# Performance work log

Measured on AMD Instinct MI355X. Metric: run time of the kernel, lower is better.

The kernel has to match this reference:

```python
import jax, jax.numpy as jnp
import numpy as np

B, T, F, H = 1024, 512, 64, 128


def setup_inputs() -> dict:
    key = jax.random.key(0)
    ks = jax.random.split(key, 9)
    s_ih = 1.0 / np.sqrt(H)
    inp = {
        "x": jax.random.normal(ks[0], (B, T, F), dtype=jnp.float32),
        # PyTorch GRU packed weights: [3H, F] and [3H, H], gate order (r, z, n)
        "W_ih": jax.random.uniform(ks[1], (3 * H, F), minval=-s_ih, maxval=s_ih, dtype=jnp.float32),
        "W_hh": jax.random.uniform(ks[2], (3 * H, H), minval=-s_ih, maxval=s_ih, dtype=jnp.float32),
        "b_ih": jax.random.uniform(ks[3], (3 * H,), minval=-s_ih, maxval=s_ih, dtype=jnp.float32),
        "b_hh": jax.random.uniform(ks[4], (3 * H,), minval=-s_ih, maxval=s_ih, dtype=jnp.float32),
        "W1": jax.random.uniform(ks[5], (32, H), minval=-1 / np.sqrt(H), maxval=1 / np.sqrt(H), dtype=jnp.float32),
        "b1": jax.random.uniform(ks[6], (32,), minval=-1 / np.sqrt(H), maxval=1 / np.sqrt(H), dtype=jnp.float32),
        "W2": jax.random.uniform(ks[7], (1, 32), minval=-1 / np.sqrt(32), maxval=1 / np.sqrt(32), dtype=jnp.float32),
        "b2": jax.random.uniform(ks[8], (1,), minval=-1 / np.sqrt(32), maxval=1 / np.sqrt(32), dtype=jnp.float32),
    }
    return inp


def _gru_last_hidden(x, W_ih, W_hh, b_ih, b_hh):
    # Precompute input-side gate pre-activations for all timesteps: [B, T, 3H]
    xg = jnp.einsum("btf,gf->btg", x, W_ih) + b_ih
    h0 = jnp.zeros((x.shape[0], W_hh.shape[1]), dtype=x.dtype)

    def step(h, xg_t):
        hg = h @ W_hh.T + b_hh  # [B, 3H]
        xr, xz, xn = jnp.split(xg_t, 3, axis=-1)
        hr, hz, hn = jnp.split(hg, 3, axis=-1)
        r = jax.nn.sigmoid(xr + hr)
        z = jax.nn.sigmoid(xz + hz)
        n = jnp.tanh(xn + r * hn)
        h_new = (1.0 - z) * n + z * h
        return h_new, None

    hT, _ = jax.lax.scan(step, h0, jnp.swapaxes(xg, 0, 1))  # scan over T
    return hT  # [B, H]


def reference(x, W_ih, W_hh, b_ih, b_hh, W1, b1, W2, b2):
    hT = _gru_last_hidden(x, W_ih, W_hh, b_ih, b_hh)
    hidden = jax.nn.relu(hT @ W1.T + b1)  # [B, 32]; dropout is identity at inference
    out = hidden @ W2.T + b2  # [B, 1]
    return out.squeeze(-1)  # [B]
```

## Files before the change

kernel.cpp:

```cpp
#include <hip/hip_runtime.h>
#include <math.h>


#define Bsz  1024
#define Tlen 512
#define Fdim 64
#define Hdim 128
#define Gdim 384
#define NB   16
#define NTHR 512
#define NBLK (Bsz / NB)

typedef __attribute__((ext_vector_type(8))) _Float16 f16x8;
typedef __attribute__((ext_vector_type(4))) _Float16 f16x4;
typedef __attribute__((ext_vector_type(2))) _Float16 f16x2;
typedef __attribute__((ext_vector_type(4))) float    f32x4;

__device__ __forceinline__ float fast_sigmoid(float v) {
    return __builtin_amdgcn_rcpf(1.f + __expf(-v));
}
__device__ __forceinline__ float fast_tanh(float v) {
    return 1.f - 2.f * __builtin_amdgcn_rcpf(__expf(2.f * v) + 1.f);
}

__global__ void
__attribute__((amdgpu_flat_work_group_size(NTHR, NTHR), amdgpu_waves_per_eu(2, 2)))
gru_mfma(const float* __restrict__ x,
         const float* __restrict__ W_ih, const float* __restrict__ W_hh,
         const float* __restrict__ b_ih, const float* __restrict__ b_hh,
         const float* __restrict__ W1, const float* __restrict__ b1,
         const float* __restrict__ W2, const float* __restrict__ b2,
         float* __restrict__ out)
{
    __shared__ __align__(16) _Float16 WH[24 * 4 * 4 * 128];
    __shared__ __align__(16) _Float16 WI[24 * 2 * 4 * 128];
    __shared__ __align__(16) _Float16 U0[6 * 4 * 16 * 8];
    __shared__ __align__(16) _Float16 U1[6 * 4 * 16 * 8];

    const int tid  = threadIdx.x;
    const int w    = tid >> 6;
    const int l    = tid & 63;
    const int q    = l >> 4;
    const int bcol = l & 15;
    const int b0   = blockIdx.x * NB;

    for (int i = tid; i < Gdim * Hdim; i += NTHR) {
        int gr = i >> 7, k = i & 127;
        int idx = (((gr >> 4) * 4 + (k >> 5)) * 4 + ((k & 31) >> 3)) * 128
                + (gr & 15) * 8 + (k & 7);
        WH[idx] = (_Float16)W_hh[i];
    }
    for (int i = tid; i < Gdim * Fdim; i += NTHR) {
        int gr = i >> 6, k = i & 63;
        int idx = (((gr >> 4) * 2 + (k >> 5)) * 4 + ((k & 31) >> 3)) * 128
                + (gr & 15) * 8 + (k & 7);
        WI[idx] = (_Float16)W_ih[i];
    }
    for (int i = tid; i < 2048; i += NTHR) U0[i] = (_Float16)0.f;
    {
        int e = tid * 2, bx_ = e >> 6, j = e & 63;
        float2 xv = *reinterpret_cast<const float2*>(
            &x[((size_t)(b0 + bx_) * Tlen + 0) * Fdim + j]);
        int kk = 128 + j;
        int idx = (((kk >> 5) * 4 + ((kk & 31) >> 3)) * 16 + bx_) * 8 + (kk & 7);
        U0[idx]     = (_Float16)xv.x;
        U0[idx + 1] = (_Float16)xv.y;
    }

    float br[4], bz[4], bnh[4], bnx[4];
    #pragma unroll
    for (int j = 0; j < 4; ++j) {
        int gr = 16 * w + q * 4 + j;
        br[j]  = b_ih[gr] + b_hh[gr];
        bz[j]  = b_ih[Hdim + gr] + b_hh[Hdim + gr];
        bnh[j] = b_hh[2 * Hdim + gr];
        bnx[j] = b_ih[2 * Hdim + gr];
    }

    float hp0 = 0.f, hp1 = 0.f, hp2 = 0.f, hp3 = 0.f;

    const int kb    = 16 * w + 4 * q;
    const int hbase = (((kb >> 5) * 4 + ((kb & 31) >> 3)) * 16 + bcol) * 8 + (kb & 7);

    const int e_x = tid * 2, bx = e_x >> 6, jx = e_x & 63;
    const int kx  = 128 + jx;
    const int xidx = (((kx >> 5) * 4 + ((kx & 31) >> 3)) * 16 + bx) * 8 + (kx & 7);
    const float* xsrc = &x[(size_t)(b0 + bx) * Tlen * Fdim + jx];

    __syncthreads();

#define WHF(gt, kt) (*reinterpret_cast<const f16x8*>(&WH[((((gt)*4+(kt))*4+q)*128) + (l&15)*8]))
#define WIF(gt, kt) (*reinterpret_cast<const f16x8*>(&WI[((((gt)*2+(kt))*4+q)*128) + (l&15)*8]))
#define MFMA(a, b, c) __builtin_amdgcn_mfma_f32_16x16x32_f16((a), (b), (c), 0, 0, 0)

    f16x8 whr0 = WHF(w, 0),      whr1 = WHF(w, 1),      whr2 = WHF(w, 2),      whr3 = WHF(w, 3);
    f16x8 whz0 = WHF(8 + w, 0),  whz1 = WHF(8 + w, 1),  whz2 = WHF(8 + w, 2),  whz3 = WHF(8 + w, 3);
    f16x8 whn0 = WHF(16 + w, 0), whn1 = WHF(16 + w, 1), whn2 = WHF(16 + w, 2), whn3 = WHF(16 + w, 3);
    f16x8 wir0 = WIF(w, 0),      wir1 = WIF(w, 1);
    f16x8 wiz0 = WIF(8 + w, 0),  wiz1 = WIF(8 + w, 1);
    f16x8 win0 = WIF(16 + w, 0), win1 = WIF(16 + w, 1);

    float2 xp = *reinterpret_cast<const float2*>(xsrc + (size_t)1 * Fdim);

    auto step = [&](const _Float16* __restrict__ Ur, _Float16* __restrict__ Uw, int t) {
        asm volatile("" : "+v"(whr0), "+v"(whr1), "+v"(whr2), "+v"(whr3),
                          "+v"(whz0), "+v"(whz1));
        asm volatile("" : "+v"(whz2), "+v"(whz3), "+v"(whn0), "+v"(whn1),
                          "+v"(whn2), "+v"(whn3));
        asm volatile("" : "+v"(wir0), "+v"(wir1), "+v"(wiz0), "+v"(wiz1),
                          "+v"(win0), "+v"(win1));

        f16x8 ub0 = *reinterpret_cast<const f16x8*>(&Ur[((0*4+q)*16 + bcol)*8]);
        f16x8 ub1 = *reinterpret_cast<const f16x8*>(&Ur[((1*4+q)*16 + bcol)*8]);
        f16x8 ub2 = *reinterpret_cast<const f16x8*>(&Ur[((2*4+q)*16 + bcol)*8]);
        f16x8 ub3 = *reinterpret_cast<const f16x8*>(&Ur[((3*4+q)*16 + bcol)*8]);
        f16x8 ub4 = *reinterpret_cast<const f16x8*>(&Ur[((4*4+q)*16 + bcol)*8]);
        f16x8 ub5 = *reinterpret_cast<const f16x8*>(&Ur[((5*4+q)*16 + bcol)*8]);

        float2 xw = xp;
        if (t + 2 < Tlen)
            xp = *reinterpret_cast<const float2*>(xsrc + (size_t)(t + 2) * Fdim);

        f32x4 cr  = {br[0],  br[1],  br[2],  br[3]};
        f32x4 cz  = {bz[0],  bz[1],  bz[2],  bz[3]};
        f32x4 cnh = {bnh[0], bnh[1], bnh[2], bnh[3]};
        f32x4 cnx = {bnx[0], bnx[1], bnx[2], bnx[3]};

        cr  = MFMA(whr0, ub0, cr);
        cz  = MFMA(whz0, ub0, cz);
        cnh = MFMA(whn0, ub0, cnh);
        cr  = MFMA(whr1, ub1, cr);
        cz  = MFMA(whz1, ub1, cz);
        cnh = MFMA(whn1, ub1, cnh);
        cr  = MFMA(whr2, ub2, cr);
        cz  = MFMA(whz2, ub2, cz);
        cnh = MFMA(whn2, ub2, cnh);
        cr  = MFMA(whr3, ub3, cr);
        cz  = MFMA(whz3, ub3, cz);
        cnh = MFMA(whn3, ub3, cnh);
        cr  = MFMA(wir0, ub4, cr);
        cz  = MFMA(wiz0, ub4, cz);
        cnx = MFMA(win0, ub4, cnx);
        cr  = MFMA(wir1, ub5, cr);
        cz  = MFMA(wiz1, ub5, cz);
        cnx = MFMA(win1, ub5, cnx);

        float r0 = fast_sigmoid(cr[0]), z0 = fast_sigmoid(cz[0]);
        float r1 = fast_sigmoid(cr[1]), z1 = fast_sigmoid(cz[1]);
        float r2 = fast_sigmoid(cr[2]), z2 = fast_sigmoid(cz[2]);
        float r3 = fast_sigmoid(cr[3]), z3 = fast_sigmoid(cz[3]);
        float n0 = fast_tanh(cnx[0] + r0 * cnh[0]);
        float n1 = fast_tanh(cnx[1] + r1 * cnh[1]);
        float n2 = fast_tanh(cnx[2] + r2 * cnh[2]);
        float n3 = fast_tanh(cnx[3] + r3 * cnh[3]);
        hp0 = (1.f - z0) * n0 + z0 * hp0;
        hp1 = (1.f - z1) * n1 + z1 * hp1;
        hp2 = (1.f - z2) * n2 + z2 * hp2;
        hp3 = (1.f - z3) * n3 + z3 * hp3;

        f16x4 hq = {(_Float16)hp0, (_Float16)hp1, (_Float16)hp2, (_Float16)hp3};
        *reinterpret_cast<f16x4*>(&Uw[hbase]) = hq;

        if (t + 1 < Tlen) {
            f16x2 xq = {(_Float16)xw.x, (_Float16)xw.y};
            *reinterpret_cast<f16x2*>(&Uw[xidx]) = xq;
        }
        __syncthreads();
    };

    #pragma unroll 1
    for (int t = 0; t < Tlen; t += 2) {
        step(U0, U1, t);
        step(U1, U0, t + 1);
    }

    {
        int m = tid & 31, b = tid >> 5;
        float acc = b1[m];
        #pragma unroll 8
        for (int k = 0; k < Hdim; ++k) {
            int ui = (((k >> 5) * 4 + ((k & 31) >> 3)) * 16 + b) * 8 + (k & 7);
            acc += W1[m * Hdim + k] * (float)U0[ui];
        }
        float v = W2[m] * fmaxf(acc, 0.f);
        v += __shfl_xor(v, 1,  32);
        v += __shfl_xor(v, 2,  32);
        v += __shfl_xor(v, 4,  32);
        v += __shfl_xor(v, 8,  32);
        v += __shfl_xor(v, 16, 32);
        if (m == 0) out[b0 + b] = v + b2[0];
    }
}

extern "C" void kernel_launch(void* const* d_in, const int* in_sizes, int n_in,
                              void* d_out, int out_size, void* d_ws, size_t ws_size,
                              hipStream_t stream)
{
    const float* x    = (const float*)d_in[0];
    const float* W_ih = (const float*)d_in[1];
    const float* W_hh = (const float*)d_in[2];
    const float* b_ih = (const float*)d_in[3];
    const float* b_hh = (const float*)d_in[4];
    const float* W1   = (const float*)d_in[5];
    const float* b1   = (const float*)d_in[6];
    const float* W2   = (const float*)d_in[7];
    const float* b2   = (const float*)d_in[8];
    float* out = (float*)d_out;

    dim3 grid(NBLK), block(NTHR);
    hipLaunchKernelGGL(gru_mfma, grid, block, 0, stream,
                       x, W_ih, W_hh, b_ih, b_hh, W1, b1, W2, b2, out);
}
```

Measured before the change: 331.3 us.

## Halve block to 4 waves, each computing two gate tiles with AGPR-held weights

Shrinks the workgroup from 8 to 4 waves, so each wave computes two 16-row gate tiles per timestep (36 MFMAs instead of 18). The recurrent weights are pinned in AGPRs to make room for the doubled register footprint, and x loads are widened to float4. The aim is to cut the per-step barrier cost and wave-scheduling overhead of the serial recurrence by using fewer, more MFMA-dense waves. The trade-off is a longer serial MFMA chain per wave and lower occupancy (waves_per_eu 1), which could lengthen each step.

```diff
diff --git a/kernel.cpp b/kernel.cpp
--- a/kernel.cpp
+++ b/kernel.cpp
@@ -8,12 +8,11 @@
 #define Hdim 128
 #define Gdim 384
 #define NB   16
-#define NTHR 512
+#define NTHR 256
 #define NBLK (Bsz / NB)
 
 typedef __attribute__((ext_vector_type(8))) _Float16 f16x8;
 typedef __attribute__((ext_vector_type(4))) _Float16 f16x4;
-typedef __attribute__((ext_vector_type(2))) _Float16 f16x2;
 typedef __attribute__((ext_vector_type(4))) float    f32x4;
 
 __device__ __forceinline__ float fast_sigmoid(float v) {
@@ -24,7 +23,7 @@
 }
 
 __global__ void
-__attribute__((amdgpu_flat_work_group_size(NTHR, NTHR), amdgpu_waves_per_eu(2, 2)))
+__attribute__((amdgpu_flat_work_group_size(NTHR, NTHR), amdgpu_waves_per_eu(1, 1)))
 gru_mfma(const float* __restrict__ x,
          const float* __restrict__ W_ih, const float* __restrict__ W_hh,
          const float* __restrict__ b_ih, const float* __restrict__ b_hh,
@@ -58,31 +57,38 @@
     }
     for (int i = tid; i < 2048; i += NTHR) U0[i] = (_Float16)0.f;
     {
-        int e = tid * 2, bx_ = e >> 6, j = e & 63;
-        float2 xv = *reinterpret_cast<const float2*>(
+        int e = tid * 4, bx_ = e >> 6, j = e & 63;
+        float4 xv = *reinterpret_cast<const float4*>(
             &x[((size_t)(b0 + bx_) * Tlen + 0) * Fdim + j]);
         int kk = 128 + j;
         int idx = (((kk >> 5) * 4 + ((kk & 31) >> 3)) * 16 + bx_) * 8 + (kk & 7);
-        U0[idx]     = (_Float16)xv.x;
-        U0[idx + 1] = (_Float16)xv.y;
-    }
-
-    float br[4], bz[4], bnh[4], bnx[4];
-    #pragma unroll
-    for (int j = 0; j < 4; ++j) {
-        int gr = 16 * w + q * 4 + j;
-        br[j]  = b_ih[gr] + b_hh[gr];
-        bz[j]  = b_ih[Hdim + gr] + b_hh[Hdim + gr];
-        bnh[j] = b_hh[2 * Hdim + gr];
-        bnx[j] = b_ih[2 * Hdim + gr];
-    }
-
-    float hp0 = 0.f, hp1 = 0.f, hp2 = 0.f, hp3 = 0.f;
-
-    const int kb    = 16 * w + 4 * q;
-    const int hbase = (((kb >> 5) * 4 + ((kb & 31) >> 3)) * 16 + bcol) * 8 + (kb & 7);
-
-    const int e_x = tid * 2, bx = e_x >> 6, jx = e_x & 63;
+        f16x4 xq = {(_Float16)xv.x, (_Float16)xv.y, (_Float16)xv.z, (_Float16)xv.w};
+        *reinterpret_cast<f16x4*>(&U0[idx]) = xq;
+    }
+
+#define GR(S, J) (16 * (2 * w + (S)) + 4 * q + (J))
+    f32x4 brv0 = {b_ih[GR(0,0)] + b_hh[GR(0,0)], b_ih[GR(0,1)] + b_hh[GR(0,1)],
+                  b_ih[GR(0,2)] + b_hh[GR(0,2)], b_ih[GR(0,3)] + b_hh[GR(0,3)]};
+    f32x4 brv1 = {b_ih[GR(1,0)] + b_hh[GR(1,0)], b_ih[GR(1,1)] + b_hh[GR(1,1)],
+                  b_ih[GR(1,2)] + b_hh[GR(1,2)], b_ih[GR(1,3)] + b_hh[GR(1,3)]};
+    f32x4 bzv0 = {b_ih[Hdim+GR(0,0)] + b_hh[Hdim+GR(0,0)], b_ih[Hdim+GR(0,1)] + b_hh[Hdim+GR(0,1)],
+                  b_ih[Hdim+GR(0,2)] + b_hh[Hdim+GR(0,2)], b_ih[Hdim+GR(0,3)] + b_hh[Hdim+GR(0,3)]};
+    f32x4 bzv1 = {b_ih[Hdim+GR(1,0)] + b_hh[Hdim+GR(1,0)], b_ih[Hdim+GR(1,1)] + b_hh[Hdim+GR(1,1)],
+                  b_ih[Hdim+GR(1,2)] + b_hh[Hdim+GR(1,2)], b_ih[Hdim+GR(1,3)] + b_hh[Hdim+GR(1,3)]};
+    f32x4 bnhv0 = {b_hh[2*Hdim+GR(0,0)], b_hh[2*Hdim+GR(0,1)], b_hh[2*Hdim+GR(0,2)], b_hh[2*Hdim+GR(0,3)]};
+    f32x4 bnhv1 = {b_hh[2*Hdim+GR(1,0)], b_hh[2*Hdim+GR(1,1)], b_hh[2*Hdim+GR(1,2)], b_hh[2*Hdim+GR(1,3)]};
+    f32x4 bnxv0 = {b_ih[2*Hdim+GR(0,0)], b_ih[2*Hdim+GR(0,1)], b_ih[2*Hdim+GR(0,2)], b_ih[2*Hdim+GR(0,3)]};
+    f32x4 bnxv1 = {b_ih[2*Hdim+GR(1,0)], b_ih[2*Hdim+GR(1,1)], b_ih[2*Hdim+GR(1,2)], b_ih[2*Hdim+GR(1,3)]};
+
+    float hp00 = 0.f, hp01 = 0.f, hp02 = 0.f, hp03 = 0.f;
+    float hp10 = 0.f, hp11 = 0.f, hp12 = 0.f, hp13 = 0.f;
+
+    const int kb0 = 16 * (2 * w + 0) + 4 * q;
+    const int kb1 = 16 * (2 * w + 1) + 4 * q;
+    const int hbase0 = (((kb0 >> 5) * 4 + ((kb0 & 31) >> 3)) * 16 + bcol) * 8 + (kb0 & 7);
+    const int hbase1 = (((kb1 >> 5) * 4 + ((kb1 & 31) >> 3)) * 16 + bcol) * 8 + (kb1 & 7);
+
+    const int e_x = tid * 4, bx = e_x >> 6, jx = e_x & 63;
     const int kx  = 128 + jx;
     const int xidx = (((kx >> 5) * 4 + ((kx & 31) >> 3)) * 16 + bx) * 8 + (kx & 7);
     const float* xsrc = &x[(size_t)(b0 + bx) * Tlen * Fdim + jx];
@@ -93,22 +99,32 @@
 #define WIF(gt, kt) (*reinterpret_cast<const f16x8*>(&WI[((((gt)*2+(kt))*4+q)*128) + (l&15)*8]))
 #define MFMA(a, b, c) __builtin_amdgcn_mfma_f32_16x16x32_f16((a), (b), (c), 0, 0, 0)
 
-    f16x8 whr0 = WHF(w, 0),      whr1 = WHF(w, 1),      whr2 = WHF(w, 2),      whr3 = WHF(w, 3);
-    f16x8 whz0 = WHF(8 + w, 0),  whz1 = WHF(8 + w, 1),  whz2 = WHF(8 + w, 2),  whz3 = WHF(8 + w, 3);
-    f16x8 whn0 = WHF(16 + w, 0), whn1 = WHF(16 + w, 1), whn2 = WHF(16 + w, 2), whn3 = WHF(16 + w, 3);
-    f16x8 wir0 = WIF(w, 0),      wir1 = WIF(w, 1);
-    f16x8 wiz0 = WIF(8 + w, 0),  wiz1 = WIF(8 + w, 1);
-    f16x8 win0 = WIF(16 + w, 0), win1 = WIF(16 + w, 1);
-
-    float2 xp = *reinterpret_cast<const float2*>(xsrc + (size_t)1 * Fdim);
+    f16x8 whr00 = WHF(2*w,      0), whr01 = WHF(2*w,      1), whr02 = WHF(2*w,      2), whr03 = WHF(2*w,      3);
+    f16x8 whr10 = WHF(2*w+1,    0), whr11 = WHF(2*w+1,    1), whr12 = WHF(2*w+1,    2), whr13 = WHF(2*w+1,    3);
+    f16x8 whz00 = WHF(8+2*w,    0), whz01 = WHF(8+2*w,    1), whz02 = WHF(8+2*w,    2), whz03 = WHF(8+2*w,    3);
+    f16x8 whz10 = WHF(8+2*w+1,  0), whz11 = WHF(8+2*w+1,  1), whz12 = WHF(8+2*w+1,  2), whz13 = WHF(8+2*w+1,  3);
+    f16x8 whn00 = WHF(16+2*w,   0), whn01 = WHF(16+2*w,   1), whn02 = WHF(16+2*w,   2), whn03 = WHF(16+2*w,   3);
+    f16x8 whn10 = WHF(16+2*w+1, 0), whn11 = WHF(16+2*w+1, 1), whn12 = WHF(16+2*w+1, 2), whn13 = WHF(16+2*w+1, 3);
+    f16x8 wir00 = WIF(2*w,      0), wir01 = WIF(2*w,      1);
+    f16x8 wir10 = WIF(2*w+1,    0), wir11 = WIF(2*w+1,    1);
+    f16x8 wiz00 = WIF(8+2*w,    0), wiz01 = WIF(8+2*w,    1);
+    f16x8 wiz10 = WIF(8+2*w+1,  0), wiz11 = WIF(8+2*w+1,  1);
+    f16x8 win00 = WIF(16+2*w,   0), win01 = WIF(16+2*w,   1);
+    f16x8 win10 = WIF(16+2*w+1, 0), win11 = WIF(16+2*w+1, 1);
+
+    float4 xp = *reinterpret_cast<const float4*>(xsrc + (size_t)1 * Fdim);
 
     auto step = [&](const _Float16* __restrict__ Ur, _Float16* __restrict__ Uw, int t) {
-        asm volatile("" : "+v"(whr0), "+v"(whr1), "+v"(whr2), "+v"(whr3),
-                          "+v"(whz0), "+v"(whz1));
-        asm volatile("" : "+v"(whz2), "+v"(whz3), "+v"(whn0), "+v"(whn1),
-                          "+v"(whn2), "+v"(whn3));
-        asm volatile("" : "+v"(wir0), "+v"(wir1), "+v"(wiz0), "+v"(wiz1),
-                          "+v"(win0), "+v"(win1));
+        asm volatile("" : "+a"(whr00), "+a"(whr01), "+a"(whr02), "+a"(whr03),
+                          "+a"(whr10), "+a"(whr11), "+a"(whr12), "+a"(whr13));
+        asm volatile("" : "+a"(whz00), "+a"(whz01), "+a"(whz02), "+a"(whz03),
+                          "+a"(whz10), "+a"(whz11), "+a"(whz12), "+a"(whz13));
+        asm volatile("" : "+a"(whn00), "+a"(whn01), "+a"(whn02), "+a"(whn03),
+                          "+a"(whn10), "+a"(whn11), "+a"(whn12), "+a"(whn13));
+        asm volatile("" : "+v"(wir00), "+v"(wir01), "+v"(wir10), "+v"(wir11),
+                          "+v"(wiz00), "+v"(wiz01));
+        asm volatile("" : "+v"(wiz10), "+v"(wiz11), "+v"(win00), "+v"(win01),
+                          "+v"(win10), "+v"(win11));
 
         f16x8 ub0 = *reinterpret_cast<const f16x8*>(&Ur[((0*4+q)*16 + bcol)*8]);
         f16x8 ub1 = *reinterpret_cast<const f16x8*>(&Ur[((1*4+q)*16 + bcol)*8]);
@@ -117,53 +133,69 @@
         f16x8 ub4 = *reinterpret_cast<const f16x8*>(&Ur[((4*4+q)*16 + bcol)*8]);
         f16x8 ub5 = *reinterpret_cast<const f16x8*>(&Ur[((5*4+q)*16 + bcol)*8]);
 
-        float2 xw = xp;
+        float4 xw = xp;
         if (t + 2 < Tlen)
-            xp = *reinterpret_cast<const float2*>(xsrc + (size_t)(t + 2) * Fdim);
-
-        f32x4 cr  = {br[0],  br[1],  br[2],  br[3]};
-        f32x4 cz  = {bz[0],  bz[1],  bz[2],  bz[3]};
-        f32x4 cnh = {bnh[0], bnh[1], bnh[2], bnh[3]};
-        f32x4 cnx = {bnx[0], bnx[1], bnx[2], bnx[3]};
-
-        cr  = MFMA(whr0, ub0, cr);
-        cz  = MFMA(whz0, ub0, cz);
-        cnh = MFMA(whn0, ub0, cnh);
-        cr  = MFMA(whr1, ub1, cr);
-        cz  = MFMA(whz1, ub1, cz);
-        cnh = MFMA(whn1, ub1, cnh);
-        cr  = MFMA(whr2, ub2, cr);
-        cz  = MFMA(whz2, ub2, cz);
-        cnh = MFMA(whn2, ub2, cnh);
-        cr  = MFMA(whr3, ub3, cr);
-        cz  = MFMA(whz3, ub3, cz);
-        cnh = MFMA(whn3, ub3, cnh);
-        cr  = MFMA(wir0, ub4, cr);
-        cz  = MFMA(wiz0, ub4, cz);
-        cnx = MFMA(win0, ub4, cnx);
-        cr  = MFMA(wir1, ub5, cr);
-        cz  = MFMA(wiz1, ub5, cz);
-        cnx = MFMA(win1, ub5, cnx);
-
-        float r0 = fast_sigmoid(cr[0]), z0 = fast_sigmoid(cz[0]);
-        float r1 = fast_sigmoid(cr[1]), z1 = fast_sigmoid(cz[1]);
-        float r2 = fast_sigmoid(cr[2]), z2 = fast_sigmoid(cz[2]);
-        float r3 = fast_sigmoid(cr[3]), z3 = fast_sigmoid(cz[3]);
-        float n0 = fast_tanh(cnx[0] + r0 * cnh[0]);
-        float n1 = fast_tanh(cnx[1] + r1 * cnh[1]);
-        float n2 = fast_tanh(cnx[2] + r2 * cnh[2]);
-        float n3 = fast_tanh(cnx[3] + r3 * cnh[3]);
-        hp0 = (1.f - z0) * n0 + z0 * hp0;
-        hp1 = (1.f - z1) * n1 + z1 * hp1;
-        hp2 = (1.f - z2) * n2 + z2 * hp2;
-        hp3 = (1.f - z3) * n3 + z3 * hp3;
-
-        f16x4 hq = {(_Float16)hp0, (_Float16)hp1, (_Float16)hp2, (_Float16)hp3};
-        *reinterpret_cast<f16x4*>(&Uw[hbase]) = hq;
+            xp = *reinterpret_cast<const float4*>(xsrc + (size_t)(t + 2) * Fdim);
+
+        f32x4 cr0 = brv0, cr1 = brv1, cz0 = bzv0, cz1 = bzv1;
+        f32x4 cnh0 = bnhv0, cnh1 = bnhv1, cnx0 = bnxv0, cnx1 = bnxv1;
+
+        cr0 = MFMA(whr00, ub0, cr0);  cr1 = MFMA(whr10, ub0, cr1);
+        cz0 = MFMA(whz00, ub0, cz0);  cz1 = MFMA(whz10, ub0, cz1);
+        cnh0 = MFMA(whn00, ub0, cnh0); cnh1 = MFMA(whn10, ub0, cnh1);
+        cr0 = MFMA(whr01, ub1, cr0);  cr1 = MFMA(whr11, ub1, cr1);
+        cz0 = MFMA(whz01, ub1, cz0);  cz1 = MFMA(whz11, ub1, cz1);
+        cnh0 = MFMA(whn01, ub1, cnh0); cnh1 = MFMA(whn11, ub1, cnh1);
+        cr0 = MFMA(whr02, ub2, cr0);  cr1 = MFMA(whr12, ub2, cr1);
+        cz0 = MFMA(whz02, ub2, cz0);  cz1 = MFMA(whz12, ub2, cz1);
+        cnh0 = MFMA(whn02, ub2, cnh0); cnh1 = MFMA(whn12, ub2, cnh1);
+        cr0 = MFMA(whr03, ub3, cr0);  cr1 = MFMA(whr13, ub3, cr1);
+        cz0 = MFMA(whz03, ub3, cz0);  cz1 = MFMA(whz13, ub3, cz1);
+        cnh0 = MFMA(whn03, ub3, cnh0); cnh1 = MFMA(whn13, ub3, cnh1);
+        cr0 = MFMA(wir00, ub4, cr0);  cr1 = MFMA(wir10, ub4, cr1);
+        cz0 = MFMA(wiz00, ub4, cz0);  cz1 = MFMA(wiz10, ub4, cz1);
+        cnx0 = MFMA(win00, ub4, cnx0); cnx1 = MFMA(win10, ub4, cnx1);
+        cr0 = MFMA(wir01, ub5, cr0);  cr1 = MFMA(wir11, ub5, cr1);
+        cz0 = MFMA(wiz01, ub5, cz0);  cz1 = MFMA(wiz11, ub5, cz1);
+        cnx0 = MFMA(win01, ub5, cnx0); cnx1 = MFMA(win11, ub5, cnx1);
+
+        {
+            float r0 = fast_sigmoid(cr0[0]), z0 = fast_sigmoid(cz0[0]);
+            float r1 = fast_sigmoid(cr0[1]), z1 = fast_sigmoid(cz0[1]);
+            float r2 = fast_sigmoid(cr0[2]), z2 = fast_sigmoid(cz0[2]);
+            float r3 = fast_sigmoid(cr0[3]), z3 = fast_sigmoid(cz0[3]);
+            float n0 = fast_tanh(cnx0[0] + r0 * cnh0[0]);
+            float n1 = fast_tanh(cnx0[1] + r1 * cnh0[1]);
+            float n2 = fast_tanh(cnx0[2] + r2 * cnh0[2]);
+            float n3 = fast_tanh(cnx0[3] + r3 * cnh0[3]);
+            hp00 = (1.f - z0) * n0 + z0 * hp00;
+            hp01 = (1.f - z1) * n1 + z1 * hp01;
+            hp02 = (1.f - z2) * n2 + z2 * hp02;
+            hp03 = (1.f - z3) * n3 + z3 * hp03;
+        }
+        {
+            float r0 = fast_sigmoid(cr1[0]), z0 = fast_sigmoid(cz1[0]);
+            float r1 = fast_sigmoid(cr1[1]), z1 = fast_sigmoid(cz1[1]);
+            float r2 = fast_sigmoid(cr1[2]), z2 = fast_sigmoid(cz1[2]);
+            float r3 = fast_sigmoid(cr1[3]), z3 = fast_sigmoid(cz1[3]);
+            float n0 = fast_tanh(cnx1[0] + r0 * cnh1[0]);
+            float n1 = fast_tanh(cnx1[1] + r1 * cnh1[1]);
+            float n2 = fast_tanh(cnx1[2] + r2 * cnh1[2]);
+            float n3 = fast_tanh(cnx1[3] + r3 * cnh1[3]);
+            hp10 = (1.f - z0) * n0 + z0 * hp10;
+            hp11 = (1.f - z1) * n1 + z1 * hp11;
+            hp12 = (1.f - z2) * n2 + z2 * hp12;
+            hp13 = (1.f - z3) * n3 + z3 * hp13;
+        }
+
+        f16x4 hq0 = {(_Float16)hp00, (_Float16)hp01, (_Float16)hp02, (_Float16)hp03};
+        f16x4 hq1 = {(_Float16)hp10, (_Float16)hp11, (_Float16)hp12, (_Float16)hp13};
+        *reinterpret_cast<f16x4*>(&Uw[hbase0]) = hq0;
+        *reinterpret_cast<f16x4*>(&Uw[hbase1]) = hq1;
 
         if (t + 1 < Tlen) {
-            f16x2 xq = {(_Float16)xw.x, (_Float16)xw.y};
-            *reinterpret_cast<f16x2*>(&Uw[xidx]) = xq;
+            f16x4 xq = {(_Float16)xw.x, (_Float16)xw.y, (_Float16)xw.z, (_Float16)xw.w};
+            *reinterpret_cast<f16x4*>(&Uw[xidx]) = xq;
         }
         __syncthreads();
     };
@@ -174,8 +206,8 @@
         step(U1, U0, t + 1);
     }
 
-    {
-        int m = tid & 31, b = tid >> 5;
+    for (int sidx = tid; sidx < 512; sidx += NTHR) {
+        int m = sidx & 31, b = sidx >> 5;
         float acc = b1[m];
         #pragma unroll 8
         for (int k = 0; k < Hdim; ++k) {
```

After: 446.2 us. 1.35x slower.

## Load GRU weights directly to registers and use LDS-only step barrier

Applied to the files above, without the earlier changes.

Weight fragments are read from global memory and converted to fp16 directly into registers, removing the shared-memory staging of W_hh and W_ih and its setup barrier work. The per-timestep __syncthreads is replaced by an s_waitcnt lgkmcnt(0) plus s_barrier wrapped in scheduling barriers, so the step no longer waits on the outstanding global prefetch of the next x slice. The hidden update is rewritten as n + z*(h-n) to save an operation. Removing the register pinning asm may let the compiler reorder or spill weight registers, and the sched barriers constrain instruction scheduling.

```diff
diff --git a/kernel.cpp b/kernel.cpp
--- a/kernel.cpp
+++ b/kernel.cpp
@@ -22,6 +22,12 @@
 __device__ __forceinline__ float fast_tanh(float v) {
     return 1.f - 2.f * __builtin_amdgcn_rcpf(__expf(2.f * v) + 1.f);
 }
+
+#define BAR_LDS() do {                                                   \
+    __builtin_amdgcn_sched_barrier(0);                                   \
+    asm volatile("s_waitcnt lgkmcnt(0)\n\ts_barrier" ::: "memory");      \
+    __builtin_amdgcn_sched_barrier(0);                                   \
+} while (0)
 
 __global__ void
 __attribute__((amdgpu_flat_work_group_size(NTHR, NTHR), amdgpu_waves_per_eu(2, 2)))
@@ -32,8 +38,6 @@
          const float* __restrict__ W2, const float* __restrict__ b2,
          float* __restrict__ out)
 {
-    __shared__ __align__(16) _Float16 WH[24 * 4 * 4 * 128];
-    __shared__ __align__(16) _Float16 WI[24 * 2 * 4 * 128];
     __shared__ __align__(16) _Float16 U0[6 * 4 * 16 * 8];
     __shared__ __align__(16) _Float16 U1[6 * 4 * 16 * 8];
 
@@ -44,18 +48,6 @@
     const int bcol = l & 15;
     const int b0   = blockIdx.x * NB;
 
-    for (int i = tid; i < Gdim * Hdim; i += NTHR) {
-        int gr = i >> 7, k = i & 127;
-        int idx = (((gr >> 4) * 4 + (k >> 5)) * 4 + ((k & 31) >> 3)) * 128
-                + (gr & 15) * 8 + (k & 7);
-        WH[idx] = (_Float16)W_hh[i];
-    }
-    for (int i = tid; i < Gdim * Fdim; i += NTHR) {
-        int gr = i >> 6, k = i & 63;
-        int idx = (((gr >> 4) * 2 + (k >> 5)) * 4 + ((k & 31) >> 3)) * 128
-                + (gr & 15) * 8 + (k & 7);
-        WI[idx] = (_Float16)W_ih[i];
-    }
     for (int i = tid; i < 2048; i += NTHR) U0[i] = (_Float16)0.f;
     {
         int e = tid * 2, bx_ = e >> 6, j = e & 63;
@@ -87,29 +79,37 @@
     const int xidx = (((kx >> 5) * 4 + ((kx & 31) >> 3)) * 16 + bx) * 8 + (kx & 7);
     const float* xsrc = &x[(size_t)(b0 + bx) * Tlen * Fdim + jx];
 
+    const int rr = l & 15;
+    auto LDWH = [&](int gt, int kt) -> f16x8 {
+        const float* p = W_hh + (size_t)(16 * gt + rr) * Hdim + kt * 32 + q * 8;
+        float4 a = *reinterpret_cast<const float4*>(p);
+        float4 b = *reinterpret_cast<const float4*>(p + 4);
+        f16x8 r = {(_Float16)a.x, (_Float16)a.y, (_Float16)a.z, (_Float16)a.w,
+                   (_Float16)b.x, (_Float16)b.y, (_Float16)b.z, (_Float16)b.w};
+        return r;
+    };
+    auto LDWI = [&](int gt, int kt) -> f16x8 {
+        const float* p = W_ih + (size_t)(16 * gt + rr) * Fdim + kt * 32 + q * 8;
+        float4 a = *reinterpret_cast<const float4*>(p);
+        float4 b = *reinterpret_cast<const float4*>(p + 4);
+        f16x8 r = {(_Float16)a.x, (_Float16)a.y, (_Float16)a.z, (_Float16)a.w,
+                   (_Float16)b.x, (_Float16)b.y, (_Float16)b.z, (_Float16)b.w};
+        return r;
+    };
+    f16x8 whr0 = LDWH(w, 0),      whr1 = LDWH(w, 1),      whr2 = LDWH(w, 2),      whr3 = LDWH(w, 3);
+    f16x8 whz0 = LDWH(8 + w, 0),  whz1 = LDWH(8 + w, 1),  whz2 = LDWH(8 + w, 2),  whz3 = LDWH(8 + w, 3);
+    f16x8 whn0 = LDWH(16 + w, 0), whn1 = LDWH(16 + w, 1), whn2 = LDWH(16 + w, 2), whn3 = LDWH(16 + w, 3);
+    f16x8 wir0 = LDWI(w, 0),      wir1 = LDWI(w, 1);
+    f16x8 wiz0 = LDWI(8 + w, 0),  wiz1 = LDWI(8 + w, 1);
+    f16x8 win0 = LDWI(16 + w, 0), win1 = LDWI(16 + w, 1);
+
     __syncthreads();
 
-#define WHF(gt, kt) (*reinterpret_cast<const f16x8*>(&WH[((((gt)*4+(kt))*4+q)*128) + (l&15)*8]))
-#define WIF(gt, kt) (*reinterpret_cast<const f16x8*>(&WI[((((gt)*2+(kt))*4+q)*128) + (l&15)*8]))
 #define MFMA(a, b, c) __builtin_amdgcn_mfma_f32_16x16x32_f16((a), (b), (c), 0, 0, 0)
 
-    f16x8 whr0 = WHF(w, 0),      whr1 = WHF(w, 1),      whr2 = WHF(w, 2),      whr3 = WHF(w, 3);
-    f16x8 whz0 = WHF(8 + w, 0),  whz1 = WHF(8 + w, 1),  whz2 = WHF(8 + w, 2),  whz3 = WHF(8 + w, 3);
-    f16x8 whn0 = WHF(16 + w, 0), whn1 = WHF(16 + w, 1), whn2 = WHF(16 + w, 2), whn3 = WHF(16 + w, 3);
-    f16x8 wir0 = WIF(w, 0),      wir1 = WIF(w, 1);
-    f16x8 wiz0 = WIF(8 + w, 0),  wiz1 = WIF(8 + w, 1);
-    f16x8 win0 = WIF(16 + w, 0), win1 = WIF(16 + w, 1);
-
     float2 xp = *reinterpret_cast<const float2*>(xsrc + (size_t)1 * Fdim);
 
     auto step = [&](const _Float16* __restrict__ Ur, _Float16* __restrict__ Uw, int t) {
-        asm volatile("" : "+v"(whr0), "+v"(whr1), "+v"(whr2), "+v"(whr3),
-                          "+v"(whz0), "+v"(whz1));
-        asm volatile("" : "+v"(whz2), "+v"(whz3), "+v"(whn0), "+v"(whn1),
-                          "+v"(whn2), "+v"(whn3));
-        asm volatile("" : "+v"(wir0), "+v"(wir1), "+v"(wiz0), "+v"(wiz1),
-                          "+v"(win0), "+v"(win1));
-
         f16x8 ub0 = *reinterpret_cast<const f16x8*>(&Ur[((0*4+q)*16 + bcol)*8]);
         f16x8 ub1 = *reinterpret_cast<const f16x8*>(&Ur[((1*4+q)*16 + bcol)*8]);
         f16x8 ub2 = *reinterpret_cast<const f16x8*>(&Ur[((2*4+q)*16 + bcol)*8]);
@@ -153,10 +153,10 @@
         float n1 = fast_tanh(cnx[1] + r1 * cnh[1]);
         float n2 = fast_tanh(cnx[2] + r2 * cnh[2]);
         float n3 = fast_tanh(cnx[3] + r3 * cnh[3]);
-        hp0 = (1.f - z0) * n0 + z0 * hp0;
-        hp1 = (1.f - z1) * n1 + z1 * hp1;
-        hp2 = (1.f - z2) * n2 + z2 * hp2;
-        hp3 = (1.f - z3) * n3 + z3 * hp3;
+        hp0 = n0 + z0 * (hp0 - n0);
+        hp1 = n1 + z1 * (hp1 - n1);
+        hp2 = n2 + z2 * (hp2 - n2);
+        hp3 = n3 + z3 * (hp3 - n3);
 
         f16x4 hq = {(_Float16)hp0, (_Float16)hp1, (_Float16)hp2, (_Float16)hp3};
         *reinterpret_cast<f16x4*>(&Uw[hbase]) = hq;
@@ -165,7 +165,7 @@
             f16x2 xq = {(_Float16)xw.x, (_Float16)xw.y};
             *reinterpret_cast<f16x2*>(&Uw[xidx]) = xq;
         }
-        __syncthreads();
+        BAR_LDS();
     };
 
     #pragma unroll 1
```

New measurement: 330.0 us. About the same (-0.4%).
